# Optimization experiments

Measured on AMD Instinct MI355X. Metric: run time of the kernel, lower is better.

Reference implementation:

```python
import jax, jax.numpy as jnp
import numpy as np

D = 256      # model_dim
H = 4        # num_heads
DPH = D // H # dim_per_head = 64
NLBL = 9     # number of per-label linear layers


def setup_inputs() -> dict:
    key0 = jax.random.key(0)
    ks = jax.random.split(key0, 16)
    N, M = 6144, 6144
    s = 1.0 / np.sqrt(D)
    inp = {
        'key':     jax.random.normal(ks[0], (N, D), jnp.float32),
        'value':   jax.random.normal(ks[1], (N, D), jnp.float32),
        'query':   jax.random.normal(ks[2], (M, D), jnp.float32),
        'label_1': jax.random.randint(ks[3], (N,), 0, NLBL),
        'label_2': jax.random.randint(ks[4], (M,), 0, NLBL),
        # 9 per-label projection weights (applied as x @ W + b)
        'Wq': jax.random.normal(ks[5], (NLBL, D, D), jnp.float32) * s,
        'bq': jax.random.normal(ks[6], (NLBL, D), jnp.float32) * 0.02,
        'Wk': jax.random.normal(ks[7], (NLBL, D, D), jnp.float32) * s,
        'bk': jax.random.normal(ks[8], (NLBL, D), jnp.float32) * 0.02,
        'Wv': jax.random.normal(ks[9], (NLBL, D, D), jnp.float32) * s,
        'bv': jax.random.normal(ks[10], (NLBL, D), jnp.float32) * 0.02,
        'Wf': jax.random.normal(ks[11], (D, D), jnp.float32) * s,
        'bf': jax.random.normal(ks[12], (D,), jnp.float32) * 0.02,
        'gamma': jnp.ones((D,), jnp.float32),
        'beta':  jnp.zeros((D,), jnp.float32),
    }
    return inp


def _label_proj(x, W, b, lbl):
    # Project every token with all 9 label weights, then pick the per-token one.
    # p: [n, 9, D]
    p = jnp.einsum('nd,ldo->nlo', x, W) + b[None]
    return jnp.take_along_axis(p, lbl[:, None, None], axis=1)[:, 0]  # [n, D]


def reference(key, value, query, label_1, label_2,
              Wq, bq, Wk, bk, Wv, bv, Wf, bf, gamma, beta):
    M = query.shape[0]
    # Per-label (dynamically routed) projections; within a group the query
    # label equals the key label, so per-token weight selection is exactly
    # the per-group loop of the original module.
    q = _label_proj(query, Wq, bq, label_2).reshape(M, H, DPH)
    k = _label_proj(key,   Wk, bk, label_1).reshape(-1, H, DPH)
    v = _label_proj(value, Wv, bv, label_1).reshape(-1, H, DPH)

    # Note: original uses scale = (dim_per_head // num_heads) ** -0.5
    scale = (DPH // H) ** (-0.5)
    scores = jnp.einsum('mhd,nhd->hmn', q, k) * scale  # [H, M, N]

    # Queries only attend to keys of the same label (block structure of
    # the original per-label gather/attention/scatter loop).
    mask = label_2[:, None] == label_1[None, :]        # [M, N]
    probs = jax.nn.softmax(jnp.where(mask[None], scores, -1e30), axis=-1)

    ctx = jnp.einsum('hmn,nhd->mhd', probs, v).reshape(M, D)
    out = ctx @ Wf + bf
    res = query + out  # residual is the unprojected query

    mu = jnp.mean(res, axis=-1, keepdims=True)
    var = jnp.var(res, axis=-1, keepdims=True)
    return (res - mu) / jnp.sqrt(var + 1e-5) * gamma + beta
```

## Files before the change

### kernel.cpp

```cpp
#include <hip/hip_runtime.h>
#include <hip/hip_bf16.h>

#define D 256
#define H 4
#define DPH 64
#define NLBL 9
#define SPLITK 4

typedef __attribute__((ext_vector_type(8))) __bf16 bf16x8;
typedef __attribute__((ext_vector_type(8))) unsigned short u16x8;
typedef __attribute__((ext_vector_type(4))) float f32x4;

__device__ __forceinline__ int sw_idx(int row, int col) {
  return row * 64 + (col ^ ((row & 7) << 3));
}

__device__ __forceinline__ unsigned int pk2(float a, float b) {
  unsigned int lo = (unsigned int)__builtin_bit_cast(unsigned short, (__bf16)a);
  unsigned int hi = (unsigned int)__builtin_bit_cast(unsigned short, (__bf16)b);
  return lo | (hi << 16);
}

__device__ __forceinline__ bf16x8 cvt8(float4 u0, float4 u1) {
  bf16x8 r;
  r[0] = (__bf16)u0.x; r[1] = (__bf16)u0.y; r[2] = (__bf16)u0.z; r[3] = (__bf16)u0.w;
  r[4] = (__bf16)u1.x; r[5] = (__bf16)u1.y; r[6] = (__bf16)u1.z; r[7] = (__bf16)u1.w;
  return r;
}

__global__ __launch_bounds__(1024) void setup_kernel(
    const int* __restrict__ lbl1, int n1, const int* __restrict__ lbl2, int n2,
    int* __restrict__ cnt, int* __restrict__ off,
    int* __restrict__ pqo, int* __restrict__ pko,
    int* __restrict__ tq, int* __restrict__ tk, int* __restrict__ ntl) {
  const int t = threadIdx.x, lane = t & 63;
  __shared__ int bins[2 * NLBL];
  if (t < 2 * NLBL) bins[t] = 0;
  __syncthreads();
  for (int a = 0; a < 2; ++a) {
    const int n = a ? n2 : n1;
    const int* lbl = a ? lbl2 : lbl1;
    for (int chunk = 0; chunk < n; chunk += 1024) {
      int i = chunk + t;
      int l = (i < n) ? lbl[i] : -1;
#pragma unroll
      for (int lab = 0; lab < NLBL; ++lab) {
        unsigned long long bal = __ballot(l == lab);
        if (lane == 0 && bal) atomicAdd(&bins[a * NLBL + lab], __popcll(bal));
      }
    }
  }
  __syncthreads();
  if (t < 2 * NLBL) cnt[t] = bins[t];
  if (t == 0) {
    int a0 = 0, a1 = 0, p0 = 0, p1 = 0, t0 = 0, t1 = 0;
    for (int l = 0; l < NLBL; ++l) {
      off[l] = a0;      a0 += bins[l];
      off[10 + l] = a1; a1 += bins[NLBL + l];
      pko[l] = p0; pqo[l] = p1;
      int tkl = (bins[l] + 63) >> 6;
      int tql = (bins[NLBL + l] + 127) >> 7;
      for (int i = 0; i < tkl; ++i) { tk[2 * t0] = l; tk[2 * t0 + 1] = p0 + (i << 6); ++t0; }
      for (int i = 0; i < tql; ++i) { tq[2 * t1] = l; tq[2 * t1 + 1] = p1 + (i << 7); ++t1; }
      p0 += tkl << 6; p1 += tql << 7;
    }
    off[9] = a0; off[19] = a1; pko[9] = p0; pqo[9] = p1;
    ntl[0] = t1; ntl[1] = t0;
  }
}

__global__ __launch_bounds__(1024) void scatter_kernel(
    const int* __restrict__ lbl1, int n1, const int* __restrict__ lbl2, int n2,
    const int* __restrict__ off, int* __restrict__ korder, int* __restrict__ qorder) {
  const int l = blockIdx.x;
  const int a = blockIdx.y;
  const int n = (a == 0) ? n1 : n2;
  const int* lbl = (a == 0) ? lbl1 : lbl2;
  int* order = (a == 0) ? korder : qorder;
  const int base = off[a * 10 + l];

  const int t = threadIdx.x, wave = t >> 6, lane = t & 63;
  __shared__ int wtot[16];
  int pos = 0;
  for (int chunk = 0; chunk < n; chunk += 1024) {
    int i = chunk + t;
    bool flag = (i < n) && (lbl[i] == l);
    unsigned long long bal = __ballot(flag);
    int wprefix = __popcll(bal & ((1ull << lane) - 1ull));
    if (lane == 0) wtot[wave] = __popcll(bal);
    __syncthreads();
    int prew = 0, tot = 0;
#pragma unroll
    for (int w = 0; w < 16; ++w) {
      prew += (w < wave) ? wtot[w] : 0;
      tot += wtot[w];
    }
    if (flag) order[base + pos + prew + wprefix] = i;
    pos += tot;
    __syncthreads();
  }
}

__global__ __launch_bounds__(256) void transW_kernel(
    const float* __restrict__ Wq, const float* __restrict__ Wk,
    const float* __restrict__ Wv, const float* __restrict__ Wf,
    __bf16* __restrict__ Wqt, __bf16* __restrict__ Wkt,
    __bf16* __restrict__ Wvt, __bf16* __restrict__ Wft) {
  int m = blockIdx.y, sub = blockIdx.x;
  const float* src; __bf16* dst;
  if (m < 9)       { src = Wq + (size_t)m * 65536;        dst = Wqt + (size_t)m * 65536; }
  else if (m < 18) { src = Wk + (size_t)(m - 9) * 65536;  dst = Wkt + (size_t)(m - 9) * 65536; }
  else if (m < 27) { src = Wv + (size_t)(m - 18) * 65536; dst = Wvt + (size_t)(m - 18) * 65536; }
  else             { src = Wf;                            dst = Wft; }
  int k0 = (sub >> 2) << 6, n0 = (sub & 3) << 6;
  __shared__ float lds[64][65];
  int t = threadIdx.x, rr = t >> 6, c = t & 63;
#pragma unroll
  for (int i = 0; i < 16; ++i) {
    int r = i * 4 + rr;
    lds[r][c] = src[(size_t)(k0 + r) * D + n0 + c];
  }
  __syncthreads();
#pragma unroll
  for (int i = 0; i < 16; ++i) {
    int r = i * 4 + rr;
    dst[(size_t)(n0 + r) * D + k0 + c] = (__bf16)lds[c][r];
  }
}

__global__ __launch_bounds__(256) void gemm_in_kernel(
    const float* __restrict__ query, const float* __restrict__ key,
    const float* __restrict__ value,
    const __bf16* __restrict__ Wqt, const __bf16* __restrict__ Wkt,
    const __bf16* __restrict__ Wvt,
    const float* __restrict__ bq, const float* __restrict__ bk,
    const float* __restrict__ bv,
    const int* __restrict__ qorder, const int* __restrict__ korder,
    const int* __restrict__ off, const int* __restrict__ cnt,
    const int* __restrict__ pqo, const int* __restrict__ pko,
    const int* __restrict__ tq, const int* __restrict__ tk,
    const int* __restrict__ ntl,
    __bf16* __restrict__ qbuf, __bf16* __restrict__ kbuf, __bf16* __restrict__ vbuf) {
  const int y = blockIdx.y;
  const int nt = (y == 0) ? ntl[0] : ntl[1];
  const int ti = (y == 0) ? ((int)blockIdx.x >> 2) : ((int)blockIdx.x >> 1);
  const int sub = (y == 0) ? ((int)blockIdx.x & 3) : ((int)blockIdx.x & 1);
  if (ti >= nt) return;
  const int* tt = (y == 0) ? tq : tk;
  const float* x = (y == 0) ? query : (y == 1 ? key : value);
  const __bf16* W = (y == 0) ? Wqt : (y == 1 ? Wkt : Wvt);
  const float* bias = (y == 0) ? bq : (y == 1 ? bk : bv);
  const int* order = (y == 0) ? qorder : korder;
  const int* po = (y == 0) ? pqo : pko;
  __bf16* outp = (y == 0) ? qbuf : (y == 1 ? kbuf : vbuf);
  const float sc = (y == 0) ? 0.36067376f : 1.0f;

  const int l = tt[2 * ti], prow0 = tt[2 * ti + 1] + sub * 32;
  const int cl = (y == 0) ? cnt[NLBL + l] : cnt[l];
  const int ooff = (y == 0) ? off[10 + l] : off[l];
  const int base = prow0 - po[l];

  const int t = threadIdx.x, w = t >> 6, lane = t & 63;
  const int lr = lane & 15, lk = lane >> 4;

  int src[2];
#pragma unroll
  for (int fi = 0; fi < 2; ++fi) {
    int ridx = base + fi * 16 + lr;
    src[fi] = (ridx < cl) ? order[ooff + ridx] : -1;
  }

  bf16x8 az;
#pragma unroll
  for (int j = 0; j < 8; ++j) az[j] = (__bf16)0.f;

  f32x4 acc[2][4];
#pragma unroll
  for (int i = 0; i < 2; ++i)
#pragma unroll
    for (int j = 0; j < 4; ++j) acc[i][j] = (f32x4){0.f, 0.f, 0.f, 0.f};

  for (int kb = 0; kb < 8; ++kb) {
    const int kbase = kb * 32 + lk * 8;
    bf16x8 a[2], b[4];
#pragma unroll
    for (int fi = 0; fi < 2; ++fi) {
      if (src[fi] >= 0) {
        const float* ap = x + (size_t)src[fi] * D + kbase;
        float4 u0 = *(const float4*)ap;
        float4 u1 = *(const float4*)(ap + 4);
        a[fi] = cvt8(u0, u1);
      } else {
        a[fi] = az;
      }
    }
#pragma unroll
    for (int fj = 0; fj < 4; ++fj) {
      int col = w * 64 + fj * 16 + lr;
      b[fj] = *(const bf16x8*)(W + (size_t)l * 65536 + (size_t)col * D + kbase);
    }
#pragma unroll
    for (int fi = 0; fi < 2; ++fi)
#pragma unroll
      for (int fj = 0; fj < 4; ++fj)
        acc[fi][fj] = __builtin_amdgcn_mfma_f32_16x16x32_bf16(a[fi], b[fj], acc[fi][fj], 0, 0, 0);
  }

#pragma unroll
  for (int fj = 0; fj < 4; ++fj) {
    int col = w * 64 + fj * 16 + lr;
    float bv_ = bias[l * D + col];
#pragma unroll
    for (int fi = 0; fi < 2; ++fi)
#pragma unroll
      for (int r = 0; r < 4; ++r) {
        int row = prow0 + fi * 16 + lk * 4 + r;
        outp[(size_t)row * D + col] = (__bf16)((acc[fi][fj][r] + bv_) * sc);
      }
  }
}

__global__ __launch_bounds__(256) void attn_mfma(
    const __bf16* __restrict__ qbuf, const __bf16* __restrict__ kbuf,
    const __bf16* __restrict__ vbuf, const int* __restrict__ cnt,
    const int* __restrict__ tq, const int* __restrict__ ntl,
    const int* __restrict__ pko,
    float* __restrict__ pctx, float* __restrict__ pstats) {
  const int tqi = blockIdx.x;
  if (tqi >= ntl[0]) return;
  const int l = tq[2 * tqi], prow0 = tq[2 * tqi + 1];
  const int h = blockIdx.y, s = blockIdx.z;
  const int nk = cnt[l];
  const int ntiles = (nk + 63) >> 6;
  const int ntsz = (ntiles + SPLITK - 1) / SPLITK;
  const int tt0 = s * ntsz;
  const int tt1 = min(ntiles, tt0 + ntsz);
  if (tt0 >= tt1) return;

  const int t = threadIdx.x;
  const int w = t >> 6, lane = t & 63;
  const int lr = lane & 15, lk = lane >> 4;

  __shared__ __align__(16) unsigned short ks[4096];
  __shared__ __align__(16) unsigned short vtl[4096];
  __shared__ __align__(16) unsigned short plds[8192];

  const int qbase = prow0 + w * 32;
  bf16x8 b_q[2][2];
#pragma unroll
  for (int qf = 0; qf < 2; ++qf)
#pragma unroll
    for (int kb = 0; kb < 2; ++kb)
      b_q[qf][kb] = *(const bf16x8*)(qbuf + (size_t)(qbase + qf * 16 + lr) * D +
                                     h * DPH + kb * 32 + lk * 8);

  f32x4 acc_o[2][4];
#pragma unroll
  for (int qf = 0; qf < 2; ++qf)
#pragma unroll
    for (int i = 0; i < 4; ++i) acc_o[qf][i] = (f32x4){0.f, 0.f, 0.f, 0.f};
  float lrun[2] = {0.f, 0.f};
  const int kb0 = pko[l];

  for (int tt = tt0; tt < tt1; ++tt) {
    const int n0 = tt << 6;
    __syncthreads();
    {
      int row = t >> 2, c0 = (t & 3) * 16;
      const uint4* kp = (const uint4*)(kbuf + (size_t)(kb0 + n0 + row) * D + h * DPH + c0);
      uint4 k0 = kp[0], k1 = kp[1];
      *(uint4*)&ks[sw_idx(row, c0)] = k0;
      *(uint4*)&ks[sw_idx(row, c0 + 8)] = k1;
    }
    {
      int key2 = (t & 31) * 2, d0 = (t >> 5) * 8;
      const unsigned short* vp = (const unsigned short*)(vbuf + (size_t)(kb0 + n0 + key2) * D + h * DPH + d0);
      u16x8 va = *(const u16x8*)vp;
      u16x8 vb = *(const u16x8*)(vp + D);
#pragma unroll
      for (int j = 0; j < 8; ++j) {
        unsigned int u = (unsigned int)va[j] | ((unsigned int)vb[j] << 16);
        *(unsigned int*)&vtl[sw_idx(d0 + j, key2)] = u;
      }
    }
    __syncthreads();

    f32x4 s_acc[2][4];
    const f32x4 zz = {0.f, 0.f, 0.f, 0.f};
#pragma unroll
    for (int fi = 0; fi < 4; ++fi) {
      bf16x8 a0 = *(const bf16x8*)&ks[sw_idx(fi * 16 + lr, lk * 8)];
#pragma unroll
      for (int qf = 0; qf < 2; ++qf)
        s_acc[qf][fi] = __builtin_amdgcn_mfma_f32_16x16x32_bf16(a0, b_q[qf][0], zz, 0, 0, 0);
    }
#pragma unroll
    for (int fi = 0; fi < 4; ++fi) {
      bf16x8 a1 = *(const bf16x8*)&ks[sw_idx(fi * 16 + lr, 32 + lk * 8)];
#pragma unroll
      for (int qf = 0; qf < 2; ++qf)
        s_acc[qf][fi] = __builtin_amdgcn_mfma_f32_16x16x32_bf16(a1, b_q[qf][1], s_acc[qf][fi], 0, 0, 0);
    }

    float p[2][16];
#pragma unroll
    for (int qf = 0; qf < 2; ++qf) {
      float ts = 0.f;
#pragma unroll
      for (int fi = 0; fi < 4; ++fi)
#pragma unroll
        for (int r = 0; r < 4; ++r) {
          int key = n0 + fi * 16 + lk * 4 + r;
          float pv = (key < nk) ? exp2f(s_acc[qf][fi][r]) : 0.f;
          p[qf][fi * 4 + r] = pv;
          ts += pv;
        }
      ts += __shfl_xor(ts, 16, 64);
      ts += __shfl_xor(ts, 32, 64);
      lrun[qf] += ts;
    }

#pragma unroll
    for (int qf = 0; qf < 2; ++qf)
#pragma unroll
      for (int fi = 0; fi < 4; ++fi) {
        unsigned int w0 = pk2(p[qf][fi * 4 + 0], p[qf][fi * 4 + 1]);
        unsigned int w1 = pk2(p[qf][fi * 4 + 2], p[qf][fi * 4 + 3]);
        int idx = w * 2048 + sw_idx(qf * 16 + lr, fi * 16 + lk * 4);
        *(uint2*)&plds[idx] = make_uint2(w0, w1);
      }

#pragma unroll
    for (int kb = 0; kb < 2; ++kb) {
      bf16x8 bp[2];
#pragma unroll
      for (int qf = 0; qf < 2; ++qf)
        bp[qf] = *(const bf16x8*)&plds[w * 2048 + sw_idx(qf * 16 + lr, kb * 32 + lk * 8)];
#pragma unroll
      for (int fi = 0; fi < 4; ++fi) {
        bf16x8 av = *(const bf16x8*)&vtl[sw_idx(fi * 16 + lr, kb * 32 + lk * 8)];
#pragma unroll
        for (int qf = 0; qf < 2; ++qf)
          acc_o[qf][fi] = __builtin_amdgcn_mfma_f32_16x16x32_bf16(av, bp[qf], acc_o[qf][fi], 0, 0, 0);
      }
    }
  }

  const size_t pbase = ((size_t)tqi * H + h) * SPLITK + s;
  float* pc = pctx + pbase * 8192;
#pragma unroll
  for (int qf = 0; qf < 2; ++qf) {
    int qloc = w * 32 + qf * 16 + lr;
#pragma unroll
    for (int fi = 0; fi < 4; ++fi)
      *(f32x4*)(pc + qloc * 64 + fi * 16 + lk * 4) = acc_o[qf][fi];
    if (lk == 0) pstats[pbase * 128 + qloc] = lrun[qf];
  }
}

__global__ __launch_bounds__(256) void proj_ln_kernel(
    const float* __restrict__ pctx, const float* __restrict__ pstats,
    const __bf16* __restrict__ Wft, const float* __restrict__ bf_,
    const float* __restrict__ query,
    const int* __restrict__ qorder, const int* __restrict__ off,
    const int* __restrict__ cnt, const int* __restrict__ pqo,
    const int* __restrict__ tq, const int* __restrict__ ntl,
    const float* __restrict__ gamma, const float* __restrict__ beta,
    float* __restrict__ out) {
  const int tqi = blockIdx.x;
  if (tqi >= ntl[0]) return;
  const int l = tq[2 * tqi];
  const int qq = blockIdx.y;
  const int prow0 = tq[2 * tqi + 1] + qq * 32;
  const int qloc0 = qq * 32;
  const int cl = cnt[NLBL + l];
  const int ooff = off[10 + l];
  const int base = prow0 - pqo[l];
  const int nk = cnt[l];
  const int ntiles = (nk + 63) >> 6;
  const int ntsz = (ntiles + SPLITK - 1) / SPLITK;
  const int nsp = ntiles ? (ntiles + ntsz - 1) / ntsz : 0;

  const int t = threadIdx.x, w = t >> 6, lane = t & 63;
  const int lr = lane & 15, lk = lane >> 4;

  __shared__ int srcs[32];
  __shared__ float linv[32][4];
  __shared__ __align__(16) unsigned short ct[32 * 256];
  __shared__ float psum[4][32], psum2[4][32];
  __shared__ float mu_s[32], is_s[32];

  if (t < 32) {
    int ridx = base + t;
    srcs[t] = (ridx < cl) ? qorder[ooff + ridx] : -1;
  }
  if (t < 128) {
    int row = t >> 2, h = t & 3;
    float L = 0.f;
    for (int s = 0; s < nsp; ++s)
      L += pstats[(((size_t)tqi * H + h) * SPLITK + s) * 128 + qloc0 + row];
    linv[row][h] = (L > 0.f) ? (1.f / L) : 0.f;
  }
  __syncthreads();

  {
    int row = t >> 3, dseg = (t & 7) * 32;
    int h = dseg >> 6, d0 = dseg & 63;
    const float* pb = pctx + (((size_t)tqi * H + h) * SPLITK) * 8192 +
                      (size_t)(qloc0 + row) * 64 + d0;
    float v[32];
#pragma unroll
    for (int j = 0; j < 32; ++j) v[j] = 0.f;
    for (int s = 0; s < nsp; ++s) {
      const float* ps = pb + (size_t)s * 8192;
#pragma unroll
      for (int j = 0; j < 32; j += 4) {
        f32x4 u = *(const f32x4*)(ps + j);
        v[j] += u[0]; v[j + 1] += u[1]; v[j + 2] += u[2]; v[j + 3] += u[3];
      }
    }
    float iv = linv[row][h];
    int xr = (row & 7) << 3;
#pragma unroll
    for (int j = 0; j < 32; j += 2)
      *(unsigned int*)&ct[row * 256 + ((dseg + j) ^ xr)] = pk2(v[j] * iv, v[j + 1] * iv);
  }
  __syncthreads();

  f32x4 acc[2][4];
#pragma unroll
  for (int i = 0; i < 2; ++i)
#pragma unroll
    for (int j = 0; j < 4; ++j) acc[i][j] = (f32x4){0.f, 0.f, 0.f, 0.f};

  for (int kb = 0; kb < 8; ++kb) {
    const int kbase = kb * 32 + lk * 8;
    bf16x8 a[2], b[4];
#pragma unroll
    for (int fi = 0; fi < 2; ++fi) {
      int row = fi * 16 + lr;
      a[fi] = *(const bf16x8*)&ct[row * 256 + (kbase ^ ((row & 7) << 3))];
    }
#pragma unroll
    for (int fj = 0; fj < 4; ++fj) {
      int col = w * 64 + fj * 16 + lr;
      b[fj] = *(const bf16x8*)(Wft + (size_t)col * D + kbase);
    }
#pragma unroll
    for (int fi = 0; fi < 2; ++fi)
#pragma unroll
      for (int fj = 0; fj < 4; ++fj)
        acc[fi][fj] = __builtin_amdgcn_mfma_f32_16x16x32_bf16(a[fi], b[fj], acc[fi][fj], 0, 0, 0);
  }

  float res[2][4][4];
  float s1[2][4], s2[2][4];
#pragma unroll
  for (int fi = 0; fi < 2; ++fi)
#pragma unroll
    for (int r = 0; r < 4; ++r) { s1[fi][r] = 0.f; s2[fi][r] = 0.f; }

#pragma unroll
  for (int fj = 0; fj < 4; ++fj) {
    int col = w * 64 + fj * 16 + lr;
    float bcol = bf_[col];
#pragma unroll
    for (int fi = 0; fi < 2; ++fi)
#pragma unroll
      for (int r = 0; r < 4; ++r) {
        int rowl = fi * 16 + lk * 4 + r;
        int sr = srcs[rowl];
        float qv = (sr >= 0) ? query[(size_t)sr * D + col] : 0.f;
        float v = acc[fi][fj][r] + bcol + qv;
        res[fi][fj][r] = v;
        s1[fi][r] += v;
        s2[fi][r] += v * v;
      }
  }

#pragma unroll
  for (int o2 = 1; o2 <= 8; o2 <<= 1) {
#pragma unroll
    for (int fi = 0; fi < 2; ++fi)
#pragma unroll
      for (int r = 0; r < 4; ++r) {
        s1[fi][r] += __shfl_xor(s1[fi][r], o2, 64);
        s2[fi][r] += __shfl_xor(s2[fi][r], o2, 64);
      }
  }
  if (lr == 0) {
#pragma unroll
    for (int fi = 0; fi < 2; ++fi)
#pragma unroll
      for (int r = 0; r < 4; ++r) {
        int rowl = fi * 16 + lk * 4 + r;
        psum[w][rowl] = s1[fi][r];
        psum2[w][rowl] = s2[fi][r];
      }
  }
  __syncthreads();
  if (t < 32) {
    float tot = psum[0][t] + psum[1][t] + psum[2][t] + psum[3][t];
    float tot2 = psum2[0][t] + psum2[1][t] + psum2[2][t] + psum2[3][t];
    float mu = tot * (1.f / D);
    float var = tot2 * (1.f / D) - mu * mu;
    mu_s[t] = mu;
    is_s[t] = rsqrtf(var + 1e-5f);
  }
  __syncthreads();

#pragma unroll
  for (int fj = 0; fj < 4; ++fj) {
    int col = w * 64 + fj * 16 + lr;
    float gc = gamma[col], bc = beta[col];
#pragma unroll
    for (int fi = 0; fi < 2; ++fi)
#pragma unroll
      for (int r = 0; r < 4; ++r) {
        int rowl = fi * 16 + lk * 4 + r;
        int sr = srcs[rowl];
        if (sr >= 0)
          out[(size_t)sr * D + col] =
              (res[fi][fj][r] - mu_s[rowl]) * is_s[rowl] * gc + bc;
      }
  }
}

extern "C" void kernel_launch(void* const* d_in, const int* in_sizes, int n_in,
                              void* d_out, int out_size, void* d_ws, size_t ws_size,
                              hipStream_t stream) {
  const float* key   = (const float*)d_in[0];
  const float* value = (const float*)d_in[1];
  const float* query = (const float*)d_in[2];
  const int*   lbl1  = (const int*)d_in[3];
  const int*   lbl2  = (const int*)d_in[4];
  const float* Wq = (const float*)d_in[5];
  const float* bq = (const float*)d_in[6];
  const float* Wk = (const float*)d_in[7];
  const float* bk = (const float*)d_in[8];
  const float* Wv = (const float*)d_in[9];
  const float* bv = (const float*)d_in[10];
  const float* Wf = (const float*)d_in[11];
  const float* bf_ = (const float*)d_in[12];
  const float* gamma = (const float*)d_in[13];
  const float* beta  = (const float*)d_in[14];
  float* out = (float*)d_out;

  const int N = in_sizes[0] / D;
  const int M = in_sizes[2] / D;
  const int MP = M + NLBL * 128;
  const int NP = N + NLBL * 64;
  const int TQCAP = (M + 127) / 128 + NLBL;
  const int TKCAP = (N + 63) / 64 + NLBL;

  int* cnt = (int*)d_ws;
  int* off = cnt + 32;
  int* pqo = off + 32;
  int* pko = pqo + 16;
  int* ntl = pko + 16;
  int* tq  = ntl + 16;
  int* tk  = tq + 2 * TQCAP;
  int* korder = tk + 2 * TKCAP;
  int* qorder = korder + N;
  size_t ihdr = (((size_t)(112 + 2 * TQCAP + 2 * TKCAP + N + M)) * 4 + 255) & ~(size_t)255;

  __bf16* Wqt = (__bf16*)((char*)d_ws + ihdr);
  __bf16* Wkt = Wqt + (size_t)9 * 65536;
  __bf16* Wvt = Wkt + (size_t)9 * 65536;
  __bf16* Wft = Wvt + (size_t)9 * 65536;
  __bf16* qbuf = Wft + 65536;
  __bf16* kbuf = qbuf + (size_t)MP * D;
  __bf16* vbuf = kbuf + (size_t)NP * D;
  float* pctx = (float*)(vbuf + (size_t)NP * D);
  float* pstats = pctx + (size_t)TQCAP * H * SPLITK * 8192;

  setup_kernel<<<1, 1024, 0, stream>>>(lbl1, N, lbl2, M, cnt, off, pqo, pko, tq, tk, ntl);

  dim3 sgrid(NLBL, 2);
  scatter_kernel<<<sgrid, 1024, 0, stream>>>(lbl1, N, lbl2, M, off, korder, qorder);

  transW_kernel<<<dim3(16, 28), 256, 0, stream>>>(Wq, Wk, Wv, Wf, Wqt, Wkt, Wvt, Wft);

  int gx = TQCAP * 4 > TKCAP * 2 ? TQCAP * 4 : TKCAP * 2;
  gemm_in_kernel<<<dim3(gx, 3), 256, 0, stream>>>(
      query, key, value, Wqt, Wkt, Wvt, bq, bk, bv,
      qorder, korder, off, cnt, pqo, pko, tq, tk, ntl, qbuf, kbuf, vbuf);

  attn_mfma<<<dim3(TQCAP, H, SPLITK), 256, 0, stream>>>(
      qbuf, kbuf, vbuf, cnt, tq, ntl, pko, pctx, pstats);

  proj_ln_kernel<<<dim3(TQCAP, 4), 256, 0, stream>>>(
      pctx, pstats, Wft, bf_, query, qorder, off, cnt, pqo, tq, ntl,
      gamma, beta, out);
}
```

Measured before the change: 105.3 us.

## Merge setup, scatter and weight transpose kernels; prefetch K/V; store partial ctx in bf16

Measured after the change: 88.92 us. -15.6%, faster.

```diff
diff --git a/kernel.cpp b/kernel.cpp
--- a/kernel.cpp
+++ b/kernel.cpp
@@ -21,6 +21,10 @@
   return lo | (hi << 16);
 }
 
+__device__ __forceinline__ float b2f(unsigned short u) {
+  return __builtin_bit_cast(float, (unsigned int)u << 16);
+}
+
 __device__ __forceinline__ bf16x8 cvt8(float4 u0, float4 u1) {
   bf16x8 r;
   r[0] = (__bf16)u0.x; r[1] = (__bf16)u0.y; r[2] = (__bf16)u0.z; r[3] = (__bf16)u0.w;
@@ -28,103 +32,123 @@
   return r;
 }
 
-__global__ __launch_bounds__(1024) void setup_kernel(
+__global__ __launch_bounds__(1024) void prep_kernel(
     const int* __restrict__ lbl1, int n1, const int* __restrict__ lbl2, int n2,
-    int* __restrict__ cnt, int* __restrict__ off,
-    int* __restrict__ pqo, int* __restrict__ pko,
-    int* __restrict__ tq, int* __restrict__ tk, int* __restrict__ ntl) {
-  const int t = threadIdx.x, lane = t & 63;
-  __shared__ int bins[2 * NLBL];
-  if (t < 2 * NLBL) bins[t] = 0;
-  __syncthreads();
-  for (int a = 0; a < 2; ++a) {
-    const int n = a ? n2 : n1;
-    const int* lbl = a ? lbl2 : lbl1;
-    for (int chunk = 0; chunk < n; chunk += 1024) {
-      int i = chunk + t;
-      int l = (i < n) ? lbl[i] : -1;
-#pragma unroll
-      for (int lab = 0; lab < NLBL; ++lab) {
-        unsigned long long bal = __ballot(l == lab);
-        if (lane == 0 && bal) atomicAdd(&bins[a * NLBL + lab], __popcll(bal));
-      }
-    }
-  }
-  __syncthreads();
-  if (t < 2 * NLBL) cnt[t] = bins[t];
-  if (t == 0) {
-    int a0 = 0, a1 = 0, p0 = 0, p1 = 0, t0 = 0, t1 = 0;
-    for (int l = 0; l < NLBL; ++l) {
-      off[l] = a0;      a0 += bins[l];
-      off[10 + l] = a1; a1 += bins[NLBL + l];
-      pko[l] = p0; pqo[l] = p1;
-      int tkl = (bins[l] + 63) >> 6;
-      int tql = (bins[NLBL + l] + 127) >> 7;
-      for (int i = 0; i < tkl; ++i) { tk[2 * t0] = l; tk[2 * t0 + 1] = p0 + (i << 6); ++t0; }
-      for (int i = 0; i < tql; ++i) { tq[2 * t1] = l; tq[2 * t1 + 1] = p1 + (i << 7); ++t1; }
-      p0 += tkl << 6; p1 += tql << 7;
-    }
-    off[9] = a0; off[19] = a1; pko[9] = p0; pqo[9] = p1;
-    ntl[0] = t1; ntl[1] = t0;
-  }
-}
-
-__global__ __launch_bounds__(1024) void scatter_kernel(
-    const int* __restrict__ lbl1, int n1, const int* __restrict__ lbl2, int n2,
-    const int* __restrict__ off, int* __restrict__ korder, int* __restrict__ qorder) {
-  const int l = blockIdx.x;
-  const int a = blockIdx.y;
-  const int n = (a == 0) ? n1 : n2;
-  const int* lbl = (a == 0) ? lbl1 : lbl2;
-  int* order = (a == 0) ? korder : qorder;
-  const int base = off[a * 10 + l];
-
-  const int t = threadIdx.x, wave = t >> 6, lane = t & 63;
-  __shared__ int wtot[16];
-  int pos = 0;
-  for (int chunk = 0; chunk < n; chunk += 1024) {
-    int i = chunk + t;
-    bool flag = (i < n) && (lbl[i] == l);
-    unsigned long long bal = __ballot(flag);
-    int wprefix = __popcll(bal & ((1ull << lane) - 1ull));
-    if (lane == 0) wtot[wave] = __popcll(bal);
-    __syncthreads();
-    int prew = 0, tot = 0;
-#pragma unroll
-    for (int w = 0; w < 16; ++w) {
-      prew += (w < wave) ? wtot[w] : 0;
-      tot += wtot[w];
-    }
-    if (flag) order[base + pos + prew + wprefix] = i;
-    pos += tot;
-    __syncthreads();
-  }
-}
-
-__global__ __launch_bounds__(256) void transW_kernel(
     const float* __restrict__ Wq, const float* __restrict__ Wk,
     const float* __restrict__ Wv, const float* __restrict__ Wf,
     __bf16* __restrict__ Wqt, __bf16* __restrict__ Wkt,
-    __bf16* __restrict__ Wvt, __bf16* __restrict__ Wft) {
-  int m = blockIdx.y, sub = blockIdx.x;
-  const float* src; __bf16* dst;
-  if (m < 9)       { src = Wq + (size_t)m * 65536;        dst = Wqt + (size_t)m * 65536; }
-  else if (m < 18) { src = Wk + (size_t)(m - 9) * 65536;  dst = Wkt + (size_t)(m - 9) * 65536; }
-  else if (m < 27) { src = Wv + (size_t)(m - 18) * 65536; dst = Wvt + (size_t)(m - 18) * 65536; }
-  else             { src = Wf;                            dst = Wft; }
-  int k0 = (sub >> 2) << 6, n0 = (sub & 3) << 6;
-  __shared__ float lds[64][65];
-  int t = threadIdx.x, rr = t >> 6, c = t & 63;
-#pragma unroll
-  for (int i = 0; i < 16; ++i) {
-    int r = i * 4 + rr;
-    lds[r][c] = src[(size_t)(k0 + r) * D + n0 + c];
-  }
-  __syncthreads();
-#pragma unroll
-  for (int i = 0; i < 16; ++i) {
-    int r = i * 4 + rr;
-    dst[(size_t)(n0 + r) * D + k0 + c] = (__bf16)lds[c][r];
+    __bf16* __restrict__ Wvt, __bf16* __restrict__ Wft,
+    int* __restrict__ cnt, int* __restrict__ off,
+    int* __restrict__ pqo, int* __restrict__ pko,
+    int* __restrict__ tq, int* __restrict__ tk, int* __restrict__ ntl,
+    int* __restrict__ korder, int* __restrict__ qorder) {
+  const int job = blockIdx.x;
+  const int t = threadIdx.x, lane = t & 63, wave = t >> 6;
+
+  __shared__ int bins[2 * NLBL];
+  __shared__ int wtot[16];
+  __shared__ float tlds[64][65];
+
+  if (job < 18) {
+    const int l = job % NLBL, a = job / NLBL;
+    const int n = a ? n2 : n1;
+    const int* lbl = a ? lbl2 : lbl1;
+    int* order = a ? qorder : korder;
+
+    if (t < NLBL) bins[t] = 0;
+    __syncthreads();
+    for (int chunk = 0; chunk < n; chunk += 1024) {
+      int i = chunk + t;
+      int lb = (i < n) ? lbl[i] : -1;
+#pragma unroll
+      for (int lab = 0; lab < NLBL; ++lab) {
+        unsigned long long bal = __ballot(lb == lab);
+        if (lane == 0 && bal) atomicAdd(&bins[lab], __popcll(bal));
+      }
+    }
+    __syncthreads();
+    int base = 0;
+#pragma unroll
+    for (int i = 0; i < NLBL; ++i) base += (i < l) ? bins[i] : 0;
+
+    int pos = 0;
+    for (int chunk = 0; chunk < n; chunk += 1024) {
+      int i = chunk + t;
+      bool flag = (i < n) && (lbl[i] == l);
+      unsigned long long bal = __ballot(flag);
+      int wprefix = __popcll(bal & ((1ull << lane) - 1ull));
+      if (lane == 0) wtot[wave] = __popcll(bal);
+      __syncthreads();
+      int prew = 0, tot = 0;
+#pragma unroll
+      for (int w = 0; w < 16; ++w) {
+        prew += (w < wave) ? wtot[w] : 0;
+        tot += wtot[w];
+      }
+      if (flag) order[base + pos + prew + wprefix] = i;
+      pos += tot;
+      __syncthreads();
+    }
+    return;
+  }
+
+  if (job == 18) {
+    if (t < 2 * NLBL) bins[t] = 0;
+    __syncthreads();
+    for (int a = 0; a < 2; ++a) {
+      const int n = a ? n2 : n1;
+      const int* lbl = a ? lbl2 : lbl1;
+      for (int chunk = 0; chunk < n; chunk += 1024) {
+        int i = chunk + t;
+        int lb = (i < n) ? lbl[i] : -1;
+#pragma unroll
+        for (int lab = 0; lab < NLBL; ++lab) {
+          unsigned long long bal = __ballot(lb == lab);
+          if (lane == 0 && bal) atomicAdd(&bins[a * NLBL + lab], __popcll(bal));
+        }
+      }
+    }
+    __syncthreads();
+    if (t < 2 * NLBL) cnt[t] = bins[t];
+    if (t == 0) {
+      int a0 = 0, a1 = 0, p0 = 0, p1 = 0, t0 = 0, t1 = 0;
+      for (int l = 0; l < NLBL; ++l) {
+        off[l] = a0;      a0 += bins[l];
+        off[10 + l] = a1; a1 += bins[NLBL + l];
+        pko[l] = p0; pqo[l] = p1;
+        int tkl = (bins[l] + 63) >> 6;
+        int tql = (bins[NLBL + l] + 127) >> 7;
+        for (int i = 0; i < tkl; ++i) { tk[2 * t0] = l; tk[2 * t0 + 1] = p0 + (i << 6); ++t0; }
+        for (int i = 0; i < tql; ++i) { tq[2 * t1] = l; tq[2 * t1 + 1] = p1 + (i << 7); ++t1; }
+        p0 += tkl << 6; p1 += tql << 7;
+      }
+      off[9] = a0; off[19] = a1; pko[9] = p0; pqo[9] = p1;
+      ntl[0] = t1; ntl[1] = t0;
+    }
+    return;
+  }
+
+  {
+    int j = job - 19;
+    int m = j >> 4, sub = j & 15;
+    const float* src; __bf16* dst;
+    if (m < 9)       { src = Wq + (size_t)m * 65536;        dst = Wqt + (size_t)m * 65536; }
+    else if (m < 18) { src = Wk + (size_t)(m - 9) * 65536;  dst = Wkt + (size_t)(m - 9) * 65536; }
+    else if (m < 27) { src = Wv + (size_t)(m - 18) * 65536; dst = Wvt + (size_t)(m - 18) * 65536; }
+    else             { src = Wf;                            dst = Wft; }
+    int k0 = (sub >> 2) << 6, n0 = (sub & 3) << 6;
+    int rr = t >> 6, c = t & 63;
+#pragma unroll
+    for (int i = 0; i < 4; ++i) {
+      int r = i * 16 + rr;
+      tlds[r][c] = src[(size_t)(k0 + r) * D + n0 + c];
+    }
+    __syncthreads();
+#pragma unroll
+    for (int i = 0; i < 4; ++i) {
+      int r = i * 16 + rr;
+      dst[(size_t)(n0 + r) * D + k0 + c] = (__bf16)tlds[c][r];
+    }
   }
 }
 
@@ -225,7 +249,7 @@
     const __bf16* __restrict__ vbuf, const int* __restrict__ cnt,
     const int* __restrict__ tq, const int* __restrict__ ntl,
     const int* __restrict__ pko,
-    float* __restrict__ pctx, float* __restrict__ pstats) {
+    __bf16* __restrict__ pctx, float* __restrict__ pstats) {
   const int tqi = blockIdx.x;
   if (tqi >= ntl[0]) return;
   const int l = tq[2 * tqi], prow0 = tq[2 * tqi + 1];
@@ -262,28 +286,35 @@
   float lrun[2] = {0.f, 0.f};
   const int kb0 = pko[l];
 
+  const int krow = t >> 2, kc0 = (t & 3) * 16;
+  const __bf16* kptr = kbuf + (size_t)(kb0 + krow) * D + h * DPH + kc0;
+  const int vkey2 = (t & 31) * 2, vd0 = (t >> 5) * 8;
+  const __bf16* vptr = vbuf + (size_t)(kb0 + vkey2) * D + h * DPH + vd0;
+
+  uint4 kreg0, kreg1;
+  u16x8 vreg0, vreg1;
+  auto LOADT = [&](int tt) {
+    const __bf16* kp = kptr + ((size_t)tt << 6) * D;
+    kreg0 = *(const uint4*)kp;
+    kreg1 = *(const uint4*)(kp + 8);
+    const __bf16* vp = vptr + ((size_t)tt << 6) * D;
+    vreg0 = *(const u16x8*)vp;
+    vreg1 = *(const u16x8*)(vp + D);
+  };
+
+  LOADT(tt0);
   for (int tt = tt0; tt < tt1; ++tt) {
     const int n0 = tt << 6;
     __syncthreads();
-    {
-      int row = t >> 2, c0 = (t & 3) * 16;
-      const uint4* kp = (const uint4*)(kbuf + (size_t)(kb0 + n0 + row) * D + h * DPH + c0);
-      uint4 k0 = kp[0], k1 = kp[1];
-      *(uint4*)&ks[sw_idx(row, c0)] = k0;
-      *(uint4*)&ks[sw_idx(row, c0 + 8)] = k1;
-    }
-    {
-      int key2 = (t & 31) * 2, d0 = (t >> 5) * 8;
-      const unsigned short* vp = (const unsigned short*)(vbuf + (size_t)(kb0 + n0 + key2) * D + h * DPH + d0);
-      u16x8 va = *(const u16x8*)vp;
-      u16x8 vb = *(const u16x8*)(vp + D);
-#pragma unroll
-      for (int j = 0; j < 8; ++j) {
-        unsigned int u = (unsigned int)va[j] | ((unsigned int)vb[j] << 16);
-        *(unsigned int*)&vtl[sw_idx(d0 + j, key2)] = u;
-      }
+    *(uint4*)&ks[sw_idx(krow, kc0)] = kreg0;
+    *(uint4*)&ks[sw_idx(krow, kc0 + 8)] = kreg1;
+#pragma unroll
+    for (int j = 0; j < 8; ++j) {
+      unsigned int u = (unsigned int)vreg0[j] | ((unsigned int)vreg1[j] << 16);
+      *(unsigned int*)&vtl[sw_idx(vd0 + j, vkey2)] = u;
     }
     __syncthreads();
+    if (tt + 1 < tt1) LOADT(tt + 1);
 
     f32x4 s_acc[2][4];
     const f32x4 zz = {0.f, 0.f, 0.f, 0.f};
@@ -347,19 +378,23 @@
   }
 
   const size_t pbase = ((size_t)tqi * H + h) * SPLITK + s;
-  float* pc = pctx + pbase * 8192;
+  __bf16* pc = pctx + pbase * 8192;
 #pragma unroll
   for (int qf = 0; qf < 2; ++qf) {
     int qloc = w * 32 + qf * 16 + lr;
 #pragma unroll
-    for (int fi = 0; fi < 4; ++fi)
-      *(f32x4*)(pc + qloc * 64 + fi * 16 + lk * 4) = acc_o[qf][fi];
+    for (int fi = 0; fi < 4; ++fi) {
+      uint2 u;
+      u.x = pk2(acc_o[qf][fi][0], acc_o[qf][fi][1]);
+      u.y = pk2(acc_o[qf][fi][2], acc_o[qf][fi][3]);
+      *(uint2*)(pc + qloc * 64 + fi * 16 + lk * 4) = u;
+    }
     if (lk == 0) pstats[pbase * 128 + qloc] = lrun[qf];
   }
 }
 
 __global__ __launch_bounds__(256) void proj_ln_kernel(
-    const float* __restrict__ pctx, const float* __restrict__ pstats,
+    const __bf16* __restrict__ pctx, const float* __restrict__ pstats,
     const __bf16* __restrict__ Wft, const float* __restrict__ bf_,
     const float* __restrict__ query,
     const int* __restrict__ qorder, const int* __restrict__ off,
@@ -406,17 +441,18 @@
   {
     int row = t >> 3, dseg = (t & 7) * 32;
     int h = dseg >> 6, d0 = dseg & 63;
-    const float* pb = pctx + (((size_t)tqi * H + h) * SPLITK) * 8192 +
-                      (size_t)(qloc0 + row) * 64 + d0;
+    const __bf16* pb = pctx + (((size_t)tqi * H + h) * SPLITK) * 8192 +
+                       (size_t)(qloc0 + row) * 64 + d0;
     float v[32];
 #pragma unroll
     for (int j = 0; j < 32; ++j) v[j] = 0.f;
     for (int s = 0; s < nsp; ++s) {
-      const float* ps = pb + (size_t)s * 8192;
-#pragma unroll
-      for (int j = 0; j < 32; j += 4) {
-        f32x4 u = *(const f32x4*)(ps + j);
-        v[j] += u[0]; v[j + 1] += u[1]; v[j + 2] += u[2]; v[j + 3] += u[3];
+      const __bf16* ps = pb + (size_t)s * 8192;
+#pragma unroll
+      for (int j4 = 0; j4 < 4; ++j4) {
+        u16x8 u = *(const u16x8*)(ps + j4 * 8);
+#pragma unroll
+        for (int e = 0; e < 8; ++e) v[j4 * 8 + e] += b2f(u[e]);
       }
     }
     float iv = linv[row][h];
@@ -571,15 +607,12 @@
   __bf16* qbuf = Wft + 65536;
   __bf16* kbuf = qbuf + (size_t)MP * D;
   __bf16* vbuf = kbuf + (size_t)NP * D;
-  float* pctx = (float*)(vbuf + (size_t)NP * D);
-  float* pstats = pctx + (size_t)TQCAP * H * SPLITK * 8192;
-
-  setup_kernel<<<1, 1024, 0, stream>>>(lbl1, N, lbl2, M, cnt, off, pqo, pko, tq, tk, ntl);
-
-  dim3 sgrid(NLBL, 2);
-  scatter_kernel<<<sgrid, 1024, 0, stream>>>(lbl1, N, lbl2, M, off, korder, qorder);
-
-  transW_kernel<<<dim3(16, 28), 256, 0, stream>>>(Wq, Wk, Wv, Wf, Wqt, Wkt, Wvt, Wft);
+  __bf16* pctx = vbuf + (size_t)NP * D;
+  float* pstats = (float*)(pctx + (size_t)TQCAP * H * SPLITK * 8192);
+
+  prep_kernel<<<19 + 28 * 16, 1024, 0, stream>>>(
+      lbl1, N, lbl2, M, Wq, Wk, Wv, Wf, Wqt, Wkt, Wvt, Wft,
+      cnt, off, pqo, pko, tq, tk, ntl, korder, qorder);
 
   int gx = TQCAP * 4 > TKCAP * 2 ? TQCAP * 4 : TKCAP * 2;
   gemm_in_kernel<<<dim3(gx, 3), 256, 0, stream>>>(
```
